# Kernel tuning notes

Measured on AMD Instinct MI355X. Metric: run time of the kernel, lower is better.

Reference implementation:

```python
import jax, jax.numpy as jnp
import numpy as np

A = 64            # n_agent == n_enemy == n_ally
MOVE = 4          # move_direction
ES = 5            # enemy_shape
ALS = 5           # ally_shape
NACT = 6          # n_actions
D = ES + ALS + NACT   # 16, transformer token dim
OBS = MOVE + ES * A + (ALS + NACT + A) * A  # 5124
B = 256


def setup_inputs() -> dict:
    key = jax.random.key(0)
    ks = jax.random.split(key, 5)
    s = 1.0 / np.sqrt(D)
    return {
        "inputs": jax.random.normal(ks[0], (B, A, OBS), dtype=jnp.float32),
        "Wq": jax.random.normal(ks[1], (D, D), dtype=jnp.float32) * s,
        "bq": jnp.zeros((D,), dtype=jnp.float32),
        "Wk": jax.random.normal(ks[2], (D, D), dtype=jnp.float32) * s,
        "bk": jnp.zeros((D,), dtype=jnp.float32),
        "Wv": jax.random.normal(ks[3], (D, D), dtype=jnp.float32) * s,
        "bv": jnp.zeros((D,), dtype=jnp.float32),
        "Wo": jax.random.normal(ks[4], (D, D), dtype=jnp.float32) * s,
        "bo": jnp.zeros((D,), dtype=jnp.float32),
    }


def reference(inputs, Wq, bq, Wk, bk, Wv, bv, Wo, bo):
    # dyn slice: skip move dirs, take enemy+ally blocks, reshape per agent,
    # keep first D=16 features of each agent row (drop the A-dim one-hot tail).
    dyn = inputs[:, :, MOVE: MOVE + ES * A + (ALS + NACT + A) * A]
    dyn = dyn.reshape(B, A, A, ES + ALS + NACT + A)[..., :D]  # [B, Ai, Atok, D]

    # single-head self-attention applied independently per (batch, agent i)
    q = dyn @ Wq + bq                                          # [B, Ai, Atok, D]
    k = dyn @ Wk + bk
    v = dyn @ Wv + bv
    scores = jnp.einsum('bitd,bisd->bits', q, k) / jnp.sqrt(jnp.float32(D))
    attn = jax.nn.softmax(scores, axis=-1)                      # [B, Ai, Atok, Atok]
    o = jnp.einsum('bits,bisd->bitd', attn, v) @ Wo + bo        # [B, Ai, Atok, D]

    # relu then sum over agent index i (the outer python loop's accumulation)
    x_sum = jax.nn.relu(o).sum(axis=1)                          # [B, Atok=A, D]

    return jnp.concatenate([inputs[:, :, :MOVE], x_sum], axis=2)  # [B, A, MOVE+D]
```

## Files before the change

### kernel.cpp

```cpp
#include <hip/hip_runtime.h>

#define NA 64
#define MOVE 4
#define OBS 5124
#define ROWS 80
#define NB 256
#define NTASK (NB * NA)
#define OUTC 20
#define WPB 4
#define NPART 16

#define WS_WQ 0
#define WS_WK 64
#define WS_WV 128
#define WS_BK 768
#define WS_BVO 784
#define WS_PART 1024

typedef __attribute__((ext_vector_type(8))) short bf16x8;
typedef __attribute__((ext_vector_type(4))) float f32x4;

__device__ __forceinline__ short f2bf(float f) {
    __bf16 h = (__bf16)f;
    return __builtin_bit_cast(short, h);
}
__device__ __forceinline__ bf16x8 mkfrag4(float a, float b, float c, float d) {
    bf16x8 t;
    t[0] = f2bf(a); t[1] = f2bf(b); t[2] = f2bf(c); t[3] = f2bf(d);
    t[4] = 0; t[5] = 0; t[6] = 0; t[7] = 0;
    return t;
}
__device__ __forceinline__ bf16x8 mkfrag8(f32x4 lo, f32x4 hi) {
    bf16x8 t;
    t[0] = f2bf(lo[0]); t[1] = f2bf(lo[1]); t[2] = f2bf(lo[2]); t[3] = f2bf(lo[3]);
    t[4] = f2bf(hi[0]); t[5] = f2bf(hi[1]); t[6] = f2bf(hi[2]); t[7] = f2bf(hi[3]);
    return t;
}

__global__ __launch_bounds__(256) void prep_kernel(
    const float* __restrict__ Wq,
    const float* __restrict__ Wk, const float* __restrict__ bk,
    const float* __restrict__ Wv, const float* __restrict__ bv,
    const float* __restrict__ Wo, const float* __restrict__ bo,
    float* __restrict__ ws)
{
    __shared__ float sWvo[256];
    const float SC = 0.36067376022224085f;
    int tid = threadIdx.x;
    {
        int e = tid >> 4, d = tid & 15;
        float acc = 0.f;
        #pragma unroll
        for (int c = 0; c < 16; ++c) acc += Wv[e * 16 + c] * Wo[c * 16 + d];
        sWvo[e * 16 + d] = acc;
    }
    __syncthreads();
    if (tid < 64) {
        int g = tid >> 4, c = tid & 15;
        bf16x8 q, k, v;
        #pragma unroll
        for (int r = 0; r < 4; ++r) {
            q[r] = f2bf(Wq[(4 * g + r) * 16 + c]);
            k[r] = f2bf(SC * Wk[(4 * g + r) * 16 + c]);
            v[r] = f2bf(sWvo[(4 * g + r) * 16 + c]);
        }
        #pragma unroll
        for (int r = 4; r < 8; ++r) { q[r] = 0; k[r] = 0; v[r] = 0; }
        ((bf16x8*)ws)[WS_WQ + tid] = q;
        ((bf16x8*)ws)[WS_WK + tid] = k;
        ((bf16x8*)ws)[WS_WV + tid] = v;
    }
    if (tid < 16) {
        ws[WS_BK + tid] = SC * bk[tid];
        float bb = bo[tid];
        #pragma unroll
        for (int c = 0; c < 16; ++c) bb += bv[c] * Wo[c * 16 + tid];
        ws[WS_BVO + tid] = bb;
    }
}

__global__ __launch_bounds__(256, 4) void attn_kernel(
    const float* __restrict__ inp,
    const float* __restrict__ bq,
    float* __restrict__ ws)
{
    __shared__ float sRed[WPB * 64 * OUTC];

    const int tid  = threadIdx.x;
    const int lane = tid & 63;
    const int w    = tid >> 6;
    const int idx  = blockIdx.x * WPB + w;
    const int g    = lane >> 4;
    const int c    = lane & 15;

    const bf16x8 wq = ((const bf16x8*)ws)[WS_WQ + lane];
    const bf16x8 wk = ((const bf16x8*)ws)[WS_WK + lane];
    const bf16x8 wv = ((const bf16x8*)ws)[WS_WV + lane];
    const float4 bq_r  = *(const float4*)(bq + 4 * g);
    const float4 bk_r  = *(const float4*)(ws + WS_BK + 4 * g);
    const float4 bvo_r = *(const float4*)(ws + WS_BVO + 4 * g);

    const float* dynp = inp + (size_t)idx * OBS + MOVE;
    bf16x8 dy[4];
    #pragma unroll
    for (int i = 0; i < 4; ++i) {
        float4 f = *(const float4*)(dynp + (16 * i + c) * ROWS + 4 * g);
        dy[i] = mkfrag4(f.x, f.y, f.z, f.w);
    }

    const f32x4 zc = {0.f, 0.f, 0.f, 0.f};

    bf16x8 qb[4], kb[4];
    f32x4 vC[4];
    #pragma unroll
    for (int i = 0; i < 4; ++i) {
        f32x4 qT = __builtin_amdgcn_mfma_f32_16x16x32_bf16(wq, dy[i], zc, 0, 0, 0);
        f32x4 kT = __builtin_amdgcn_mfma_f32_16x16x32_bf16(wk, dy[i], zc, 0, 0, 0);
        vC[i]    = __builtin_amdgcn_mfma_f32_16x16x32_bf16(dy[i], wv, zc, 0, 0, 0);
        qb[i] = mkfrag4(qT[0] + bq_r.x, qT[1] + bq_r.y, qT[2] + bq_r.z, qT[3] + bq_r.w);
        kb[i] = mkfrag4(kT[0] + bk_r.x, kT[1] + bk_r.y, kT[2] + bk_r.z, kT[3] + bk_r.w);
    }
    const bf16x8 vb_lo = mkfrag8(vC[0], vC[1]);
    const bf16x8 vb_hi = mkfrag8(vC[2], vC[3]);

    #pragma unroll
    for (int j = 0; j < 4; ++j) {
        f32x4 s0 = __builtin_amdgcn_mfma_f32_16x16x32_bf16(kb[0], qb[j], zc, 0, 0, 0);
        f32x4 s1 = __builtin_amdgcn_mfma_f32_16x16x32_bf16(kb[1], qb[j], zc, 0, 0, 0);
        f32x4 s2 = __builtin_amdgcn_mfma_f32_16x16x32_bf16(kb[2], qb[j], zc, 0, 0, 0);
        f32x4 s3 = __builtin_amdgcn_mfma_f32_16x16x32_bf16(kb[3], qb[j], zc, 0, 0, 0);

        float part = 0.f;
        #pragma unroll
        for (int r = 0; r < 4; ++r) {
            s0[r] = __builtin_amdgcn_exp2f(s0[r]); part += s0[r];
            s1[r] = __builtin_amdgcn_exp2f(s1[r]); part += s1[r];
            s2[r] = __builtin_amdgcn_exp2f(s2[r]); part += s2[r];
            s3[r] = __builtin_amdgcn_exp2f(s3[r]); part += s3[r];
        }
        part += __shfl_xor(part, 16);
        part += __shfl_xor(part, 32);
        float inv = __builtin_amdgcn_rcpf(part);

        bf16x8 p_lo = mkfrag8(s0, s1);
        bf16x8 p_hi = mkfrag8(s2, s3);

        f32x4 ot;
        ot = __builtin_amdgcn_mfma_f32_16x16x32_bf16(vb_lo, p_lo, zc, 0, 0, 0);
        ot = __builtin_amdgcn_mfma_f32_16x16x32_bf16(vb_hi, p_hi, ot, 0, 0, 0);

        float4 st;
        st.x = fmaxf(fmaf(ot[0], inv, bvo_r.x), 0.f);
        st.y = fmaxf(fmaf(ot[1], inv, bvo_r.y), 0.f);
        st.z = fmaxf(fmaf(ot[2], inv, bvo_r.z), 0.f);
        st.w = fmaxf(fmaf(ot[3], inv, bvo_r.w), 0.f);
        *(float4*)(&sRed[(w * 64 + 16 * j + c) * OUTC + 4 * g]) = st;
    }

    __syncthreads();

    {
        int t = tid >> 2, dq = tid & 3;
        const float4 a0 = *(const float4*)(&sRed[(0 * 64 + t) * OUTC + dq * 4]);
        const float4 a1 = *(const float4*)(&sRed[(1 * 64 + t) * OUTC + dq * 4]);
        const float4 a2 = *(const float4*)(&sRed[(2 * 64 + t) * OUTC + dq * 4]);
        const float4 a3 = *(const float4*)(&sRed[(3 * 64 + t) * OUTC + dq * 4]);
        float4 st;
        st.x = a0.x + a1.x + a2.x + a3.x;
        st.y = a0.y + a1.y + a2.y + a3.y;
        st.z = a0.z + a1.z + a2.z + a3.z;
        st.w = a0.w + a1.w + a2.w + a3.w;
        *(float4*)(ws + WS_PART + (size_t)blockIdx.x * 1024 + t * 16 + dq * 4) = st;
    }
}

__global__ __launch_bounds__(256) void reduce_kernel(
    const float* __restrict__ inp, const float* __restrict__ ws,
    float* __restrict__ out)
{
    const int b   = blockIdx.x;
    const int tid = threadIdx.x;
    const float* pb = ws + WS_PART + (size_t)b * (NPART * 1024);

    if (tid < 64) {
        float4 mv = *(const float4*)(inp + ((size_t)b * NA + tid) * OBS);
        *(float4*)(out + ((size_t)b * NA + tid) * OUTC) = mv;
    }
    #pragma unroll
    for (int r = 0; r < 4; ++r) {
        int e = tid + r * 256;
        float s = 0.f;
        #pragma unroll
        for (int p = 0; p < NPART; ++p) s += pb[p * 1024 + e];
        int t = e >> 4, d = e & 15;
        out[((size_t)b * NA + t) * OUTC + MOVE + d] = s;
    }
}

extern "C" void kernel_launch(void* const* d_in, const int* in_sizes, int n_in,
                              void* d_out, int out_size, void* d_ws, size_t ws_size,
                              hipStream_t stream) {
    const float* inp = (const float*)d_in[0];
    const float* Wq  = (const float*)d_in[1];
    const float* bq  = (const float*)d_in[2];
    const float* Wk  = (const float*)d_in[3];
    const float* bk  = (const float*)d_in[4];
    const float* Wv  = (const float*)d_in[5];
    const float* bv  = (const float*)d_in[6];
    const float* Wo  = (const float*)d_in[7];
    const float* bo  = (const float*)d_in[8];
    float* out = (float*)d_out;
    float* ws  = (float*)d_ws;

    hipLaunchKernelGGL(prep_kernel, dim3(1), dim3(256), 0, stream, Wq, Wk, bk, Wv, bv, Wo, bo, ws);
    hipLaunchKernelGGL(attn_kernel, dim3(NTASK / WPB), dim3(256), 0, stream, inp, bq, ws);
    hipLaunchKernelGGL(reduce_kernel, dim3(NB), dim3(256), 0, stream, inp, ws, out);
}
```

Baseline: 45.50 us.

## Double waves per block, halve partials, move move-dir copy into attention kernel

Each attention block now runs 8 waves (512 threads), so it reduces 8 agents in LDS before writing a partial, which halves the per-batch partials the reduce kernel must sum. The move-direction copy moves from the reduce kernel into the attention kernel, and the dyn loads become nontemporal. The reduce kernel now reads and writes float4s. LDS per block doubles to about 40KB, which may limit how many blocks fit on a CU.

After: 46.39 us. No clear change (+2.0%).

```diff
diff --git a/kernel.cpp b/kernel.cpp
--- a/kernel.cpp
+++ b/kernel.cpp
@@ -7,8 +7,8 @@
 #define NB 256
 #define NTASK (NB * NA)
 #define OUTC 20
-#define WPB 4
-#define NPART 16
+#define WPB 8
+#define NPART 8
 
 #define WS_WQ 0
 #define WS_WK 64
@@ -79,10 +79,11 @@
     }
 }
 
-__global__ __launch_bounds__(256, 4) void attn_kernel(
+__global__ __launch_bounds__(512, 4) void attn_kernel(
     const float* __restrict__ inp,
     const float* __restrict__ bq,
-    float* __restrict__ ws)
+    float* __restrict__ ws,
+    float* __restrict__ out)
 {
     __shared__ float sRed[WPB * 64 * OUTC];
 
@@ -100,12 +101,18 @@
     const float4 bk_r  = *(const float4*)(ws + WS_BK + 4 * g);
     const float4 bvo_r = *(const float4*)(ws + WS_BVO + 4 * g);
 
+    if (lane == 0) {
+        float4 mv = *(const float4*)(inp + (size_t)idx * OBS);
+        *(float4*)(out + (size_t)idx * OUTC) = mv;
+    }
+
     const float* dynp = inp + (size_t)idx * OBS + MOVE;
     bf16x8 dy[4];
     #pragma unroll
     for (int i = 0; i < 4; ++i) {
-        float4 f = *(const float4*)(dynp + (16 * i + c) * ROWS + 4 * g);
-        dy[i] = mkfrag4(f.x, f.y, f.z, f.w);
+        f32x4 f = __builtin_nontemporal_load(
+            (const f32x4*)(dynp + (16 * i + c) * ROWS + 4 * g));
+        dy[i] = mkfrag4(f[0], f[1], f[2], f[3]);
     }
 
     const f32x4 zc = {0.f, 0.f, 0.f, 0.f};
@@ -159,42 +166,34 @@
 
     __syncthreads();
 
-    {
+    if (tid < 256) {
         int t = tid >> 2, dq = tid & 3;
-        const float4 a0 = *(const float4*)(&sRed[(0 * 64 + t) * OUTC + dq * 4]);
-        const float4 a1 = *(const float4*)(&sRed[(1 * 64 + t) * OUTC + dq * 4]);
-        const float4 a2 = *(const float4*)(&sRed[(2 * 64 + t) * OUTC + dq * 4]);
-        const float4 a3 = *(const float4*)(&sRed[(3 * 64 + t) * OUTC + dq * 4]);
-        float4 st;
-        st.x = a0.x + a1.x + a2.x + a3.x;
-        st.y = a0.y + a1.y + a2.y + a3.y;
-        st.z = a0.z + a1.z + a2.z + a3.z;
-        st.w = a0.w + a1.w + a2.w + a3.w;
+        float4 st = make_float4(0.f, 0.f, 0.f, 0.f);
+        #pragma unroll
+        for (int ww = 0; ww < WPB; ++ww) {
+            const float4 a = *(const float4*)(&sRed[(ww * 64 + t) * OUTC + dq * 4]);
+            st.x += a.x; st.y += a.y; st.z += a.z; st.w += a.w;
+        }
         *(float4*)(ws + WS_PART + (size_t)blockIdx.x * 1024 + t * 16 + dq * 4) = st;
     }
 }
 
 __global__ __launch_bounds__(256) void reduce_kernel(
-    const float* __restrict__ inp, const float* __restrict__ ws,
-    float* __restrict__ out)
+    const float* __restrict__ ws, float* __restrict__ out)
 {
     const int b   = blockIdx.x;
     const int tid = threadIdx.x;
     const float* pb = ws + WS_PART + (size_t)b * (NPART * 1024);
 
-    if (tid < 64) {
-        float4 mv = *(const float4*)(inp + ((size_t)b * NA + tid) * OBS);
-        *(float4*)(out + ((size_t)b * NA + tid) * OUTC) = mv;
-    }
-    #pragma unroll
-    for (int r = 0; r < 4; ++r) {
-        int e = tid + r * 256;
-        float s = 0.f;
-        #pragma unroll
-        for (int p = 0; p < NPART; ++p) s += pb[p * 1024 + e];
-        int t = e >> 4, d = e & 15;
-        out[((size_t)b * NA + t) * OUTC + MOVE + d] = s;
-    }
+    int e4 = tid * 4;
+    float4 s = make_float4(0.f, 0.f, 0.f, 0.f);
+    #pragma unroll
+    for (int p = 0; p < NPART; ++p) {
+        const float4 a = *(const float4*)(pb + p * 1024 + e4);
+        s.x += a.x; s.y += a.y; s.z += a.z; s.w += a.w;
+    }
+    int t = e4 >> 4, d = e4 & 15;
+    *(float4*)(out + ((size_t)b * NA + t) * OUTC + MOVE + d) = s;
 }
 
 extern "C" void kernel_launch(void* const* d_in, const int* in_sizes, int n_in,
@@ -213,6 +212,6 @@
     float* ws  = (float*)d_ws;
 
     hipLaunchKernelGGL(prep_kernel, dim3(1), dim3(256), 0, stream, Wq, Wk, bk, Wv, bv, Wo, bo, ws);
-    hipLaunchKernelGGL(attn_kernel, dim3(NTASK / WPB), dim3(256), 0, stream, inp, bq, ws);
-    hipLaunchKernelGGL(reduce_kernel, dim3(NB), dim3(256), 0, stream, inp, ws, out);
-}
+    hipLaunchKernelGGL(attn_kernel, dim3(NTASK / WPB), dim3(512), 0, stream, inp, bq, ws, out);
+    hipLaunchKernelGGL(reduce_kernel, dim3(NB), dim3(256), 0, stream, ws, out);
+}
```
